# Optimization experiments

Measured on AMD Instinct MI355X. Metric: run time of the kernel, lower is better.

Reference implementation:

```python
import jax, jax.numpy as jnp
import numpy as np

N = 50000      # nodes
E = 800000     # edges (before self-loops)
F_IN = 128     # num_features
HID = 32       # hidden channels per head (conv1)
HEADS = 4      # conv1 heads
C = 40         # classes (conv2 out channels)
OUT_HEADS = 1  # conv2 heads
NEG_SLOPE = 0.2


def setup_inputs() -> dict:
    key = jax.random.key(0)
    ks = jax.random.split(key, 10)
    x = jax.random.normal(ks[0], (N, F_IN), jnp.float32)
    edge_index = jax.random.randint(ks[1], (2, E), 0, N, jnp.int32)
    s1 = 1.0 / np.sqrt(F_IN).astype(np.float32)
    s1h = 1.0 / np.sqrt(HID).astype(np.float32)
    s2 = 1.0 / np.sqrt(HEADS * HID).astype(np.float32)
    s2c = 1.0 / np.sqrt(C).astype(np.float32)
    W1 = jax.random.normal(ks[2], (F_IN, HEADS * HID), jnp.float32) * s1
    att_src1 = jax.random.normal(ks[3], (HEADS, HID), jnp.float32) * s1h
    att_dst1 = jax.random.normal(ks[4], (HEADS, HID), jnp.float32) * s1h
    bias1 = jnp.zeros((HEADS * HID,), jnp.float32)
    W2 = jax.random.normal(ks[5], (HEADS * HID, OUT_HEADS * C), jnp.float32) * s2
    att_src2 = jax.random.normal(ks[6], (OUT_HEADS, C), jnp.float32) * s2c
    att_dst2 = jax.random.normal(ks[7], (OUT_HEADS, C), jnp.float32) * s2c
    bias2 = jnp.zeros((C,), jnp.float32)
    return {"x": x, "edge_index": edge_index,
            "W1": W1, "att_src1": att_src1, "att_dst1": att_dst1, "bias1": bias1,
            "W2": W2, "att_src2": att_src2, "att_dst2": att_dst2, "bias2": bias2}


def gat_layer(h_in, src, dst, W, a_src, a_dst, bias, heads, out_ch, concat):
    """PyG GATConv (v1) in inference mode (no dropout on attention)."""
    n = h_in.shape[0]
    h = (h_in @ W).reshape(n, heads, out_ch)              # [N,H,F]
    e_src = jnp.einsum('nhf,hf->nh', h, a_src)            # [N,H]
    e_dst = jnp.einsum('nhf,hf->nh', h, a_dst)            # [N,H]
    alpha = jax.nn.leaky_relu(e_src[src] + e_dst[dst], NEG_SLOPE)  # [E,H]
    # segment softmax over destination-node neighborhoods
    amax = jax.ops.segment_max(alpha, dst, num_segments=n)
    amax = jnp.where(jnp.isfinite(amax), amax, 0.0)
    ex = jnp.exp(alpha - amax[dst])
    denom = jax.ops.segment_sum(ex, dst, num_segments=n)
    coef = ex / (denom[dst] + 1e-16)                      # [E,H]
    # scatter-aggregate weighted source messages
    out = jax.ops.segment_sum(h[src] * coef[:, :, None], dst, num_segments=n)  # [N,H,F]
    out = out.reshape(n, heads * out_ch) if concat else out.mean(axis=1)
    return out + bias


def reference(x, edge_index, W1, att_src1, att_dst1, bias1, W2, att_src2, att_dst2, bias2):
    n = x.shape[0]
    loop = jnp.arange(n, dtype=edge_index.dtype)          # GATConv adds self-loops
    src = jnp.concatenate([edge_index[0], loop])
    dst = jnp.concatenate([edge_index[1], loop])
    h = jax.nn.elu(gat_layer(x, src, dst, W1, att_src1, att_dst1, bias1, HEADS, HID, True))
    out = gat_layer(h, src, dst, W2, att_src2, att_dst2, bias2, OUT_HEADS, C, False)
    return (jax.nn.log_softmax(out, axis=1), jax.nn.softmax(out, axis=1))
```

## Files before the change

kernel.cpp:

```cpp
#include <hip/hip_runtime.h>
#include <hip/hip_bf16.h>

#define F1   128
#define H1   4
#define C2   40
#define NEG  0.2f
#define BN   16
#define DS   96

typedef __hip_bfloat16 bf16;
typedef float f32x2 __attribute__((ext_vector_type(2)));

__device__ __forceinline__ float ldf(const void* p, size_t i, int isbf) {
    return isbf ? __bfloat162float(((const bf16*)p)[i]) : ((const float*)p)[i];
}
__device__ __forceinline__ float lrelu(float a) { return a > 0.f ? a : NEG * a; }

__device__ __forceinline__ void up2(unsigned g, float& lo, float& hi) {
    lo = __uint_as_float(g << 16);
    hi = __uint_as_float(g & 0xffff0000u);
}
__device__ __forceinline__ f32x2 up2v(unsigned g) {
    f32x2 r;
    r.x = __uint_as_float(g << 16);
    r.y = __uint_as_float(g & 0xffff0000u);
    return r;
}

__global__ void k_prep(const unsigned short* __restrict__ x, int* __restrict__ deg,
                       int N, int* __restrict__ flag) {
    int i = blockIdx.x * 256 + threadIdx.x;
    if (i < N) deg[i] = 0;
    if (blockIdx.x == 0) {
        __shared__ int sh[256];
        int cnt = 0;
        for (int k = threadIdx.x; k < 8192; k += 256)
            if (((x[k] >> 7) & 0xFF) >= 160) cnt++;
        sh[threadIdx.x] = cnt;
        __syncthreads();
        for (int s = 128; s > 0; s >>= 1) {
            if (threadIdx.x < s) sh[threadIdx.x] += sh[threadIdx.x + s];
            __syncthreads();
        }
        if (threadIdx.x == 0) flag[0] = (sh[0] < 100) ? 1 : 0;
    }
}

__global__ void k_gemm1(const void* __restrict__ x, const void* __restrict__ W1,
                        const void* __restrict__ as1, const void* __restrict__ ad1,
                        const int* __restrict__ flag, const int* __restrict__ ei,
                        int E, int ET, int* __restrict__ deg, int* __restrict__ ebuf2,
                        bf16* __restrict__ h1b, float* __restrict__ es1,
                        float* __restrict__ ed1, int N) {
    int per = (ET + gridDim.x - 1) / gridDim.x;
    int he0 = blockIdx.x * per;
    int he1 = he0 + per; if (he1 > ET) he1 = ET;
    for (int e = he0 + threadIdx.x; e < he1; e += 256) {
        int s, d;
        if (e < E) { s = ei[e]; d = ei[E + e]; }
        else       { s = e - E; d = e - E; }
        int pos = atomicAdd(&deg[d], 1);
        if (pos < DS) ebuf2[d * DS + pos] = s;
    }
    __shared__ float xs[BN][F1];
    const int isbf = flag[0];
    int n0 = blockIdx.x * BN, t = threadIdx.x;
    for (int i = t; i < BN * F1; i += 256) {
        int nn = i >> 7, kk = i & 127;
        int n = n0 + nn; if (n >= N) n = N - 1;
        xs[nn][kk] = ldf(x, (size_t)n * F1 + kk, isbf);
    }
    __syncthreads();
    int col = t & 127, nh = t >> 7;
    float a[8] = {0.f, 0.f, 0.f, 0.f, 0.f, 0.f, 0.f, 0.f};
    if (isbf) {
        const bf16* W = (const bf16*)W1;
#pragma unroll 2
        for (int k = 0; k < F1; k += 4) {
            float w0 = __bfloat162float(W[(size_t)k * F1 + col]);
            float w1 = __bfloat162float(W[(size_t)(k + 1) * F1 + col]);
            float w2 = __bfloat162float(W[(size_t)(k + 2) * F1 + col]);
            float w3 = __bfloat162float(W[(size_t)(k + 3) * F1 + col]);
#pragma unroll
            for (int j = 0; j < 8; j++) {
                float4 xv = *(const float4*)&xs[nh + 2 * j][k];
                a[j] = fmaf(xv.x, w0, a[j]);
                a[j] = fmaf(xv.y, w1, a[j]);
                a[j] = fmaf(xv.z, w2, a[j]);
                a[j] = fmaf(xv.w, w3, a[j]);
            }
        }
    } else {
        const float* W = (const float*)W1;
#pragma unroll 2
        for (int k = 0; k < F1; k += 4) {
            float w0 = W[(size_t)k * F1 + col];
            float w1 = W[(size_t)(k + 1) * F1 + col];
            float w2 = W[(size_t)(k + 2) * F1 + col];
            float w3 = W[(size_t)(k + 3) * F1 + col];
#pragma unroll
            for (int j = 0; j < 8; j++) {
                float4 xv = *(const float4*)&xs[nh + 2 * j][k];
                a[j] = fmaf(xv.x, w0, a[j]);
                a[j] = fmaf(xv.y, w1, a[j]);
                a[j] = fmaf(xv.z, w2, a[j]);
                a[j] = fmaf(xv.w, w3, a[j]);
            }
        }
    }
    float asv = ldf(as1, col, isbf), adv = ldf(ad1, col, isbf);
    int h = col >> 5;
#pragma unroll
    for (int j = 0; j < 8; j++) {
        int n = n0 + nh + 2 * j;
        float s = a[j] * asv, dd = a[j] * adv;
#pragma unroll
        for (int off = 16; off > 0; off >>= 1) {
            s += __shfl_down(s, off, 32);
            dd += __shfl_down(dd, off, 32);
        }
        if (n < N) {
            h1b[(size_t)n * F1 + col] = __float2bfloat16(a[j]);
            if ((t & 31) == 0) { es1[n * H1 + h] = s; ed1[n * H1 + h] = dd; }
        }
    }
}

__global__ void __launch_bounds__(256) k_l1(
        const int* __restrict__ deg, const int* __restrict__ ebuf2,
        const float* __restrict__ es1, const float* __restrict__ ed1,
        const uint4* __restrict__ h1p4, const void* __restrict__ b1,
        const void* __restrict__ W2, const void* __restrict__ as2,
        const void* __restrict__ ad2, const int* __restrict__ flag,
        bf16* __restrict__ h2b, float* __restrict__ es2, float* __restrict__ ed2,
        int N) {
    int w = threadIdx.x >> 6, l = threadIdx.x & 63;
    int d = blockIdx.x * 4 + w; if (d >= N) d = N - 1;
    int cnt = deg[d]; if (cnt > DS) cnt = DS;
    int start = d * DS, end = start + cnt;
    int q = l >> 4, c16 = l & 15, h = c16 >> 2;
    float edh = ed1[d * H1 + h];
    f32x2 acc[4] = {{0.f, 0.f}, {0.f, 0.f}, {0.f, 0.f}, {0.f, 0.f}};
    float dsum = 0.f;

    auto body = [&](int base) {
        int e_i = base + q;
        int s = ebuf2[e_i];
        float esv = es1[s * H1 + h];
        uint4 g = h1p4[(size_t)s * 16 + c16];
        float ev = __expf(lrelu(esv + edh));
        f32x2 ev2 = {ev, ev};
        acc[0] += ev2 * up2v(g.x);
        acc[1] += ev2 * up2v(g.y);
        acc[2] += ev2 * up2v(g.z);
        acc[3] += ev2 * up2v(g.w);
        dsum += ev;
    };

    int i = start;
    for (; i + 12 <= end; i += 12) { body(i); body(i + 4); body(i + 8); }
    for (; i + 4 <= end; i += 4) body(i);
    if (i < end && i + q < end) body(i);

#pragma unroll
    for (int off = 16; off <= 32; off <<= 1) {
#pragma unroll
        for (int j = 0; j < 4; j++) {
            acc[j].x += __shfl_xor(acc[j].x, off, 64);
            acc[j].y += __shfl_xor(acc[j].y, off, 64);
        }
        dsum += __shfl_xor(dsum, off, 64);
    }

    const int isbf = flag[0];
    __shared__ float hs[4][F1];
    if (q == 0) {
        float inv = 1.f / (dsum + 1e-16f);
#pragma unroll
        for (int j = 0; j < 8; j++) {
            int col = c16 * 8 + j;
            float av = (j & 1) ? acc[j >> 1].y : acc[j >> 1].x;
            float v = av * inv + ldf(b1, col, isbf);
            hs[w][col] = v > 0.f ? v : (__expf(v) - 1.f);
        }
    }
    __syncthreads();
    float a2 = 0.f;
    if (l < C2) {
        if (isbf) {
            const bf16* W = (const bf16*)W2;
#pragma unroll 8
            for (int k = 0; k < F1; k++)
                a2 = fmaf(hs[w][k], __bfloat162float(W[(size_t)k * C2 + l]), a2);
        } else {
            const float* W = (const float*)W2;
#pragma unroll 8
            for (int k = 0; k < F1; k++) a2 = fmaf(hs[w][k], W[(size_t)k * C2 + l], a2);
        }
        h2b[(size_t)d * C2 + l] = __float2bfloat16(a2);
    }
    float ps = (l < C2) ? a2 * ldf(as2, l, isbf) : 0.f;
    float pd = (l < C2) ? a2 * ldf(ad2, l, isbf) : 0.f;
#pragma unroll
    for (int off = 32; off > 0; off >>= 1) {
        ps += __shfl_xor(ps, off, 64);
        pd += __shfl_xor(pd, off, 64);
    }
    if (l == 0) { es2[d] = ps; ed2[d] = pd; }
}

__global__ void __launch_bounds__(256) k_l2(
        const int* __restrict__ deg, const int* __restrict__ ebuf2,
        const float* __restrict__ es2, const float* __restrict__ ed2,
        const unsigned* __restrict__ h2p, const void* __restrict__ b2,
        const int* __restrict__ flag, void* __restrict__ out, int N) {
    int w = threadIdx.x >> 6, l = threadIdx.x & 63;
    int d = blockIdx.x * 4 + w; if (d >= N) d = N - 1;
    int cnt = deg[d]; if (cnt > DS) cnt = DS;
    int start = d * DS, end = start + cnt;
    float edd = ed2[d];
    int half = l >> 5, j = l & 31;
    float acc0 = 0.f, acc1 = 0.f, dsum = 0.f;

    auto proc1 = [&](int e) {
        int s = ebuf2[e];
        float xv = __expf(lrelu(es2[s] + edd));
        if (j < 20) {
            float lo, hi; up2(h2p[(size_t)s * 20 + j], lo, hi);
            acc0 = fmaf(xv, lo, acc0); acc1 = fmaf(xv, hi, acc1);
        }
        dsum += xv;
    };

    int i = start;
    for (; i + 8 <= end; i += 8) {
        int b = i + half * 4;
        int s0 = ebuf2[b], s1 = ebuf2[b + 1], s2 = ebuf2[b + 2], s3 = ebuf2[b + 3];
        float x0 = __expf(lrelu(es2[s0] + edd));
        float x1 = __expf(lrelu(es2[s1] + edd));
        float x2 = __expf(lrelu(es2[s2] + edd));
        float x3 = __expf(lrelu(es2[s3] + edd));
        if (j < 20) {
            unsigned g0 = h2p[(size_t)s0 * 20 + j], g1 = h2p[(size_t)s1 * 20 + j];
            unsigned g2 = h2p[(size_t)s2 * 20 + j], g3 = h2p[(size_t)s3 * 20 + j];
            float lo, hi;
            up2(g0, lo, hi); acc0 = fmaf(x0, lo, acc0); acc1 = fmaf(x0, hi, acc1);
            up2(g1, lo, hi); acc0 = fmaf(x1, lo, acc0); acc1 = fmaf(x1, hi, acc1);
            up2(g2, lo, hi); acc0 = fmaf(x2, lo, acc0); acc1 = fmaf(x2, hi, acc1);
            up2(g3, lo, hi); acc0 = fmaf(x3, lo, acc0); acc1 = fmaf(x3, hi, acc1);
        }
        dsum += (x0 + x1) + (x2 + x3);
    }
    for (; i + 2 <= end; i += 2) proc1(i + half);
    if (i < end && half == 0) proc1(i);

    acc0 += __shfl_xor(acc0, 32, 64);
    acc1 += __shfl_xor(acc1, 32, 64);
    dsum += __shfl_xor(dsum, 32, 64);

    const int isbf = flag[0];
    float inv = 1.f / (dsum + 1e-16f);
    float v0 = -1e30f, v1 = -1e30f;
    if (l < 20) {
        v0 = acc0 * inv + ldf(b2, 2 * l, isbf);
        v1 = acc1 * inv + ldf(b2, 2 * l + 1, isbf);
    }
    float m = fmaxf(v0, v1);
#pragma unroll
    for (int off = 16; off > 0; off >>= 1) m = fmaxf(m, __shfl_xor(m, off, 32));
    float sv = (l < 20) ? __expf(v0 - m) + __expf(v1 - m) : 0.f;
#pragma unroll
    for (int off = 16; off > 0; off >>= 1) sv += __shfl_xor(sv, off, 32);
    float lse = m + __logf(sv);
    if (l < 20) {
        float ls0 = v0 - lse, ls1 = v1 - lse;
        size_t base = (size_t)d * C2 + 2 * l, halfo = (size_t)N * C2;
        if (isbf) {
            bf16* o = (bf16*)out;
            o[base] = __float2bfloat16(ls0);
            o[base + 1] = __float2bfloat16(ls1);
            o[halfo + base] = __float2bfloat16(__expf(ls0));
            o[halfo + base + 1] = __float2bfloat16(__expf(ls1));
        } else {
            float* o = (float*)out;
            o[base] = ls0;
            o[base + 1] = ls1;
            o[halfo + base] = __expf(ls0);
            o[halfo + base + 1] = __expf(ls1);
        }
    }
}

extern "C" void kernel_launch(void* const* d_in, const int* in_sizes, int n_in,
                              void* d_out, int out_size, void* d_ws, size_t ws_size,
                              hipStream_t stream) {
    const int N  = in_sizes[0] / F1;
    const int E  = in_sizes[1] / 2;
    const int ET = E + N;
    const int NB = (N + 255) / 256;

    const void* x   = d_in[0];
    const int*  ei  = (const int*)d_in[1];
    const void* W1  = d_in[2];
    const void* as1 = d_in[3];
    const void* ad1 = d_in[4];
    const void* b1  = d_in[5];
    const void* W2  = d_in[6];
    const void* as2 = d_in[7];
    const void* ad2 = d_in[8];
    const void* b2  = d_in[9];

    float* ws = (float*)d_ws;
    auto al4 = [](size_t v) { return (v + 3) & ~(size_t)3; };
    size_t o = 0;
    bf16*  h1b  = (bf16*)(ws + o); o = al4(o + (size_t)64 * N);
    float* es1  = ws + o; o = al4(o + (size_t)H1 * N);
    float* ed1  = ws + o; o = al4(o + (size_t)H1 * N);
    bf16*  h2b  = (bf16*)(ws + o); o = al4(o + (size_t)20 * N);
    float* es2  = ws + o; o = al4(o + N);
    float* ed2  = ws + o; o = al4(o + N);
    int*   deg  = (int*)(ws + o); o = al4(o + N);
    int*   flag = (int*)(ws + o); o = al4(o + 4);
    int*   ebuf2 = (int*)(ws + o); o = al4(o + (size_t)DS * N);

    k_prep<<<NB, 256, 0, stream>>>((const unsigned short*)x, deg, N, flag);
    k_gemm1<<<(N + BN - 1) / BN, 256, 0, stream>>>(x, W1, as1, ad1, flag, ei, E, ET,
                                                   deg, ebuf2, h1b, es1, ed1, N);
    k_l1<<<(N + 3) / 4, 256, 0, stream>>>(deg, ebuf2, es1, ed1, (const uint4*)h1b,
                                          b1, W2, as2, ad2, flag, h2b, es2, ed2, N);
    k_l2<<<(N + 3) / 4, 256, 0, stream>>>(deg, ebuf2, es2, ed2, (const unsigned*)h2b,
                                          b2, flag, d_out, N);
}
```

Before: 290.8 us.

## Precompute per-edge attention weights into LDS before gathering neighbor features

Both aggregation kernels now run a first phase with one lane per incoming edge. That phase loads the source index, computes the exp'd leaky-relu attention weight for all heads, stores both in shared memory and reduces the denominator with wave shuffles. The gather loop then reads indices and weights from LDS instead of having every lane group recompute exp and reload es/ebuf. The hs buffer in layer 1 is padded to reduce LDS bank conflicts in the W2 matvec. This adds a block-level sync, extra LDS use and padded-lane work when the degree is not a multiple of 16.

```diff
diff --git a/kernel.cpp b/kernel.cpp
--- a/kernel.cpp
+++ b/kernel.cpp
@@ -137,43 +137,79 @@
     int w = threadIdx.x >> 6, l = threadIdx.x & 63;
     int d = blockIdx.x * 4 + w; if (d >= N) d = N - 1;
     int cnt = deg[d]; if (cnt > DS) cnt = DS;
-    int start = d * DS, end = start + cnt;
+    int start = d * DS;
+
+    __shared__ int   s_sh[4][DS];
+    __shared__ float ev_sh[4][4][DS + 4];
+    __shared__ float hs[4][144];
+
+    float4 edv = *(const float4*)&ed1[(size_t)d * 4];
+    float t0 = 0.f, t1 = 0.f, t2 = 0.f, t3 = 0.f;
+    if (l < cnt) {
+        int s = ebuf2[start + l];
+        s_sh[w][l] = s;
+        float4 es4 = *(const float4*)&es1[(size_t)s * 4];
+        float v0 = __expf(lrelu(es4.x + edv.x));
+        float v1 = __expf(lrelu(es4.y + edv.y));
+        float v2 = __expf(lrelu(es4.z + edv.z));
+        float v3 = __expf(lrelu(es4.w + edv.w));
+        ev_sh[w][0][l] = v0; ev_sh[w][1][l] = v1;
+        ev_sh[w][2][l] = v2; ev_sh[w][3][l] = v3;
+        t0 = v0; t1 = v1; t2 = v2; t3 = v3;
+    }
+    if (cnt > 64) {
+        int l2 = 64 + l;
+        if (l2 < cnt) {
+            int s = ebuf2[start + l2];
+            s_sh[w][l2] = s;
+            float4 es4 = *(const float4*)&es1[(size_t)s * 4];
+            float v0 = __expf(lrelu(es4.x + edv.x));
+            float v1 = __expf(lrelu(es4.y + edv.y));
+            float v2 = __expf(lrelu(es4.z + edv.z));
+            float v3 = __expf(lrelu(es4.w + edv.w));
+            ev_sh[w][0][l2] = v0; ev_sh[w][1][l2] = v1;
+            ev_sh[w][2][l2] = v2; ev_sh[w][3][l2] = v3;
+            t0 += v0; t1 += v1; t2 += v2; t3 += v3;
+        }
+    }
+#pragma unroll
+    for (int off = 32; off > 0; off >>= 1) {
+        t0 += __shfl_xor(t0, off, 64);
+        t1 += __shfl_xor(t1, off, 64);
+        t2 += __shfl_xor(t2, off, 64);
+        t3 += __shfl_xor(t3, off, 64);
+    }
+    __syncthreads();
+
     int q = l >> 4, c16 = l & 15, h = c16 >> 2;
-    float edh = ed1[d * H1 + h];
     f32x2 acc[4] = {{0.f, 0.f}, {0.f, 0.f}, {0.f, 0.f}, {0.f, 0.f}};
-    float dsum = 0.f;
-
-    auto body = [&](int base) {
-        int e_i = base + q;
-        int s = ebuf2[e_i];
-        float esv = es1[s * H1 + h];
-        uint4 g = h1p4[(size_t)s * 16 + c16];
-        float ev = __expf(lrelu(esv + edh));
-        f32x2 ev2 = {ev, ev};
-        acc[0] += ev2 * up2v(g.x);
-        acc[1] += ev2 * up2v(g.y);
-        acc[2] += ev2 * up2v(g.z);
-        acc[3] += ev2 * up2v(g.w);
-        dsum += ev;
-    };
-
-    int i = start;
-    for (; i + 12 <= end; i += 12) { body(i); body(i + 4); body(i + 8); }
-    for (; i + 4 <= end; i += 4) body(i);
-    if (i < end && i + q < end) body(i);
+    for (int i = 0; i < cnt; i += 16) {
+#pragma unroll
+        for (int u = 0; u < 4; u++) {
+            int e = i + q + 4 * u;
+            int ec = min(e, cnt - 1);
+            float evh = (e < cnt) ? ev_sh[w][h][ec] : 0.f;
+            int s = s_sh[w][ec];
+            uint4 g = h1p4[(size_t)s * 16 + c16];
+            f32x2 ev2 = {evh, evh};
+            acc[0] += ev2 * up2v(g.x);
+            acc[1] += ev2 * up2v(g.y);
+            acc[2] += ev2 * up2v(g.z);
+            acc[3] += ev2 * up2v(g.w);
+        }
+    }
 
 #pragma unroll
     for (int off = 16; off <= 32; off <<= 1) {
 #pragma unroll
-        for (int j = 0; j < 4; j++) {
-            acc[j].x += __shfl_xor(acc[j].x, off, 64);
-            acc[j].y += __shfl_xor(acc[j].y, off, 64);
-        }
-        dsum += __shfl_xor(dsum, off, 64);
+        for (int jj = 0; jj < 4; jj++) {
+            acc[jj].x += __shfl_xor(acc[jj].x, off, 64);
+            acc[jj].y += __shfl_xor(acc[jj].y, off, 64);
+        }
     }
 
     const int isbf = flag[0];
-    __shared__ float hs[4][F1];
+    float dsum = (h == 0) ? t0 : (h == 1) ? t1 : (h == 2) ? t2 : t3;
     if (q == 0) {
         float inv = 1.f / (dsum + 1e-16f);
 #pragma unroll
@@ -181,7 +217,7 @@
             int col = c16 * 8 + j;
             float av = (j & 1) ? acc[j >> 1].y : acc[j >> 1].x;
             float v = av * inv + ldf(b1, col, isbf);
-            hs[w][col] = v > 0.f ? v : (__expf(v) - 1.f);
+            hs[w][col + (col >> 3)] = v > 0.f ? v : (__expf(v) - 1.f);
         }
     }
     __syncthreads();
@@ -191,11 +227,12 @@
             const bf16* W = (const bf16*)W2;
 #pragma unroll 8
             for (int k = 0; k < F1; k++)
-                a2 = fmaf(hs[w][k], __bfloat162float(W[(size_t)k * C2 + l]), a2);
+                a2 = fmaf(hs[w][k + (k >> 3)], __bfloat162float(W[(size_t)k * C2 + l]), a2);
         } else {
             const float* W = (const float*)W2;
 #pragma unroll 8
-            for (int k = 0; k < F1; k++) a2 = fmaf(hs[w][k], W[(size_t)k * C2 + l], a2);
+            for (int k = 0; k < F1; k++)
+                a2 = fmaf(hs[w][k + (k >> 3)], W[(size_t)k * C2 + l], a2);
         }
         h2b[(size_t)d * C2 + l] = __float2bfloat16(a2);
     }
@@ -217,46 +254,53 @@
     int w = threadIdx.x >> 6, l = threadIdx.x & 63;
     int d = blockIdx.x * 4 + w; if (d >= N) d = N - 1;
     int cnt = deg[d]; if (cnt > DS) cnt = DS;
-    int start = d * DS, end = start + cnt;
+    int start = d * DS;
     float edd = ed2[d];
+
+    __shared__ int   s_sh2[4][DS];
+    __shared__ float x_sh[4][DS];
+
+    float xv = 0.f;
+    if (l < cnt) {
+        int s = ebuf2[start + l];
+        s_sh2[w][l] = s;
+        xv = __expf(lrelu(es2[s] + edd));
+        x_sh[w][l] = xv;
+    }
+    float dsum = xv;
+    if (cnt > 64) {
+        int l2 = 64 + l;
+        if (l2 < cnt) {
+            int s = ebuf2[start + l2];
+            s_sh2[w][l2] = s;
+            float x2 = __expf(lrelu(es2[s] + edd));
+            x_sh[w][l2] = x2;
+            dsum += x2;
+        }
+    }
+#pragma unroll
+    for (int off = 32; off > 0; off >>= 1) dsum += __shfl_xor(dsum, off, 64);
+    __syncthreads();
+
     int half = l >> 5, j = l & 31;
-    float acc0 = 0.f, acc1 = 0.f, dsum = 0.f;
-
-    auto proc1 = [&](int e) {
-        int s = ebuf2[e];
-        float xv = __expf(lrelu(es2[s] + edd));
-        if (j < 20) {
-            float lo, hi; up2(h2p[(size_t)s * 20 + j], lo, hi);
-            acc0 = fmaf(xv, lo, acc0); acc1 = fmaf(xv, hi, acc1);
-        }
-        dsum += xv;
-    };
-
-    int i = start;
-    for (; i + 8 <= end; i += 8) {
-        int b = i + half * 4;
-        int s0 = ebuf2[b], s1 = ebuf2[b + 1], s2 = ebuf2[b + 2], s3 = ebuf2[b + 3];
-        float x0 = __expf(lrelu(es2[s0] + edd));
-        float x1 = __expf(lrelu(es2[s1] + edd));
-        float x2 = __expf(lrelu(es2[s2] + edd));
-        float x3 = __expf(lrelu(es2[s3] + edd));
-        if (j < 20) {
-            unsigned g0 = h2p[(size_t)s0 * 20 + j], g1 = h2p[(size_t)s1 * 20 + j];
-            unsigned g2 = h2p[(size_t)s2 * 20 + j], g3 = h2p[(size_t)s3 * 20 + j];
-            float lo, hi;
-            up2(g0, lo, hi); acc0 = fmaf(x0, lo, acc0); acc1 = fmaf(x0, hi, acc1);
-            up2(g1, lo, hi); acc0 = fmaf(x1, lo, acc0); acc1 = fmaf(x1, hi, acc1);
-            up2(g2, lo, hi); acc0 = fmaf(x2, lo, acc0); acc1 = fmaf(x2, hi, acc1);
-            up2(g3, lo, hi); acc0 = fmaf(x3, lo, acc0); acc1 = fmaf(x3, hi, acc1);
-        }
-        dsum += (x0 + x1) + (x2 + x3);
-    }
-    for (; i + 2 <= end; i += 2) proc1(i + half);
-    if (i < end && half == 0) proc1(i);
-
-    acc0 += __shfl_xor(acc0, 32, 64);
-    acc1 += __shfl_xor(acc1, 32, 64);
-    dsum += __shfl_xor(dsum, 32, 64);
+    float acc0 = 0.f, acc1 = 0.f;
+    if (j < 20) {
+        for (int i = 0; i < cnt; i += 16) {
+#pragma unroll
+            for (int u = 0; u < 8; u++) {
+                int e = i + half * 8 + u;
+                int ec = min(e, cnt - 1);
+                float x = (e < cnt) ? x_sh[w][ec] : 0.f;
+                int s = s_sh2[w][ec];
+                unsigned g = h2p[(size_t)s * 20 + j];
+                float lo, hi; up2(g, lo, hi);
+                acc0 = fmaf(x, lo, acc0);
+                acc1 = fmaf(x, hi, acc1);
+            }
+        }
+        acc0 += __shfl_xor(acc0, 32, 64);
+        acc1 += __shfl_xor(acc1, 32, 64);
+    }
 
     const int isbf = flag[0];
     float inv = 1.f / (dsum + 1e-16f);
```

Measured after the change: 286.0 us. No clear change (-1.6%).
